# Performance work log

Hardware: AMD Instinct MI355X
Metric: run time of the kernel (lower is better)

## Reference

```python
import math
import jax, jax.numpy as jnp
import numpy as np

H = 12   # num attention heads
DH = 64  # head dim
K = 2    # pooling kernel
ST = 2   # pooling stride


def _alibi_slopes(n):
    def pow2_slopes(n):
        start = 2 ** (-2 ** (-(math.log2(n) - 3)))
        return [start * (start ** i) for i in range(n)]
    if math.log2(n).is_integer():
        return pow2_slopes(n)
    c = 2 ** math.floor(math.log2(n))
    return pow2_slopes(c) + _alibi_slopes(2 * c)[0::2][: n - c]


def _alibi_bias(p, s):
    # [1, H, p, s]; -slope * |i - j|
    rel = np.abs(np.arange(s)[None, :] - np.arange(p)[:, None]).astype(np.float32)
    slopes = np.asarray(_alibi_slopes(H), dtype=np.float32)
    return jnp.asarray((-slopes[:, None, None] * rel[None])[None])


def masked_avg_pool(x, mask):
    # x: [b, S, d] float, mask: [b, S] bool
    b, S, d = x.shape
    pad = (K - S) if K > S else (S - K) % ST
    if pad:
        x = jnp.pad(x, ((0, 0), (0, pad), (0, 0)))
        mask = jnp.pad(mask, ((0, 0), (0, pad)))
    p = (S + pad - K) // ST + 1
    idx = jnp.arange(p)[:, None] * ST + jnp.arange(K)[None, :]  # [p, K]
    xb = x[:, idx]        # [b, p, K, d]
    mb = mask[:, idx]     # [b, p, K]
    norm = jnp.maximum(mb.sum(-1), 1).astype(x.dtype)  # [b, p]
    y = (xb * mb[..., None].astype(x.dtype)).sum(-2) / norm[..., None]
    return y, mb.any(-1)


def setup_inputs() -> dict:
    key = jax.random.key(0)
    k1, k2, k3, k4 = jax.random.split(key, 4)
    B, S, D = 64, 512, 768
    return {
        "hidden_states": jax.random.normal(k1, (B, S, D), dtype=jnp.float32),
        "attention_mask": jax.random.randint(k2, (B, S), 0, 2, dtype=jnp.int32),
        "Wqkv_w": jax.random.normal(k3, (D, 3 * D), dtype=jnp.float32) * 0.02,
        "Wqkv_b": jax.random.normal(k4, (3 * D,), dtype=jnp.float32) * 0.02,
    }


def reference(hidden_states, attention_mask, Wqkv_w, Wqkv_b):
    mask = attention_mask.astype(bool)                    # [b, s]
    b, s, _ = hidden_states.shape
    # fused QKV proj; repad() zeroes padded rows
    qkv = (hidden_states @ Wqkv_w + Wqkv_b) * mask[..., None].astype(hidden_states.dtype)
    q, k, v = jnp.split(qkv, 3, axis=-1)                  # each [b, s, H*DH]
    # masked avg pooling of queries (flattened heads, as in the module)
    q_pooled, new_mask = masked_avg_pool(q, mask)         # [b, p, H*DH], [b, p]
    p = q_pooled.shape[1]
    qh = q_pooled.reshape(b, p, H, DH).transpose(0, 2, 1, 3)  # [b, H, p, DH]
    kh = k.reshape(b, s, H, DH).transpose(0, 2, 1, 3)         # [b, H, s, DH]
    vh = v.reshape(b, s, H, DH).transpose(0, 2, 1, 3)
    # additive bias: 0 where both query and key valid, else -10000; plus ALiBi
    pair = new_mask[:, :, None] & mask[:, None, :]            # [b, p, s]
    bias = jnp.where(pair, 0.0, -10000.0)[:, None] + _alibi_bias(p, s)  # [b, H, p, s]
    scores = jnp.einsum("bhpd,bhsd->bhps", qh, kh) / math.sqrt(DH) + bias
    attn = jax.nn.softmax(scores, axis=-1)
    out = jnp.einsum("bhps,bhsd->bhpd", attn, vh)             # [b, H, p, DH]
    attn_output = out.transpose(0, 2, 1, 3).reshape(b, p, H * DH)
    nm = new_mask[..., None].astype(attn_output.dtype)
    attn_output = attn_output * nm        # emulate unpad(): zero invalid rows
    residual_query = q_pooled * nm
    return attn_output, new_mask, residual_query
```

## Files before the change

kernel.cpp:

```cpp
#include <hip/hip_runtime.h>
#include <cstdint>
#include <cstddef>

#define HH 12
#define DHD 64
#define BB 64
#define SS 512
#define DD 768
#define PP 256
#define N3 2304

typedef __attribute__((ext_vector_type(8))) short bf16x8_t;
typedef __attribute__((ext_vector_type(4))) float f32x4_t;

__constant__ float c_slopes[12] = {
  0.5f, 0.25f, 0.125f, 0.0625f, 0.03125f, 0.015625f, 0.0078125f, 0.00390625f,
  0.70710678118654752f, 0.35355339059327376f, 0.17677669529663688f, 0.08838834764831844f
};

__device__ __forceinline__ ushort f2bf(float f) {
  union { float f; unsigned u; } v; v.f = f;
  unsigned r = v.u + 0x7fffu + ((v.u >> 16) & 1u);
  return (ushort)(r >> 16);
}
__device__ __forceinline__ float bf2f(ushort u) {
  union { unsigned u; float f; } v; v.u = ((unsigned)u) << 16;
  return v.f;
}
__device__ __forceinline__ void gload_lds16(const ushort* g, ushort* l) {
  __builtin_amdgcn_global_load_lds(
      (const __attribute__((address_space(1))) void*)g,
      (__attribute__((address_space(3))) void*)l, 16, 0, 0);
}

__global__ void cast_hs_kernel(const float* __restrict__ in, ushort* __restrict__ out) {
  int i = blockIdx.x * 256 + threadIdx.x;
  float4 v = ((const float4*)in)[i];
  ushort4 o;
  o.x = f2bf(v.x); o.y = f2bf(v.y); o.z = f2bf(v.z); o.w = f2bf(v.w);
  ((ushort4*)out)[i] = o;
}

__global__ void transpose_w_kernel(const float* __restrict__ W, ushort* __restrict__ Wt) {
  __shared__ float tile[32][33];
  int n0 = blockIdx.x * 32, k0 = blockIdx.y * 32;
  int tx = threadIdx.x & 31, ty = threadIdx.x >> 5;
  for (int r = ty; r < 32; r += 8) tile[r][tx] = W[(size_t)(k0 + r) * N3 + n0 + tx];
  __syncthreads();
  for (int r = ty; r < 32; r += 8) Wt[(size_t)(n0 + r) * DD + k0 + tx] = f2bf(tile[tx][r]);
}

__global__ __launch_bounds__(512, 2) void gemm_qkv_kernel(
    const ushort* __restrict__ A, const ushort* __restrict__ Wt,
    const float* __restrict__ bias, const int* __restrict__ mask,
    ushort* __restrict__ qkv) {
  __shared__ __align__(16) ushort As[2][16384];
  __shared__ __align__(16) ushort Bs[2][16384];
  const int wg = blockIdx.x;
  const int swz = (wg & 7) * 144 + (wg >> 3);
  const int bm = (swz / 9) * 256;
  const int bn = (swz % 9) * 256;
  const int tid = threadIdx.x;
  const int lane = tid & 63;
  const int wave = tid >> 6;
  const int wm = (wave >> 2) * 128;
  const int wn = (wave & 3) * 64;
  const int fr = lane & 15, quad = lane >> 4;
  const int xr = (fr & 7) << 3;
  const int q8 = quad * 8;

  const int rsub = tid >> 3;
  const int cg8 = ((tid & 7) ^ (rsub & 7)) * 8;
  const ushort* Ag = A  + (size_t)(bm + rsub) * DD + cg8;
  const ushort* Bg = Wt + (size_t)(bn + rsub) * DD + cg8;
  ushort* AsW = &As[0][0] + wave * 512;
  ushort* BsW = &Bs[0][0] + wave * 512;

  f32x4_t acc[8][4];
#pragma unroll
  for (int i = 0; i < 8; i++)
#pragma unroll
    for (int j = 0; j < 4; j++) acc[i][j] = (f32x4_t){0.f, 0.f, 0.f, 0.f};

#pragma unroll
  for (int l = 0; l < 4; l++) {
    gload_lds16(Ag + (size_t)l * 64 * DD,      AsW + l * 4096);
    gload_lds16(Bg + (size_t)l * 64 * DD,      BsW + l * 4096);
  }
#pragma unroll
  for (int l = 0; l < 4; l++) {
    gload_lds16(Ag + (size_t)l * 64 * DD + 64, AsW + 16384 + l * 4096);
    gload_lds16(Bg + (size_t)l * 64 * DD + 64, BsW + 16384 + l * 4096);
  }
  asm volatile("s_waitcnt vmcnt(8)" ::: "memory");
  __builtin_amdgcn_s_barrier();

#pragma unroll 2
  for (int t = 0; t < 12; t++) {
    const ushort* Ab = &As[t & 1][0];
    const ushort* Bb = &Bs[t & 1][0];
    bf16x8_t a[4][2], b0[2][2], b1[2][2];
#pragma unroll
    for (int m = 0; m < 4; m++)
#pragma unroll
      for (int kk = 0; kk < 2; kk++)
        a[m][kk] = *(const bf16x8_t*)&Ab[(wm + m * 16 + fr) * 64 + ((kk * 32 + q8) ^ xr)];
#pragma unroll
    for (int n = 0; n < 2; n++)
#pragma unroll
      for (int kk = 0; kk < 2; kk++)
        b0[n][kk] = *(const bf16x8_t*)&Bb[(wn + n * 16 + fr) * 64 + ((kk * 32 + q8) ^ xr)];
    asm volatile("" ::: "memory");
    __builtin_amdgcn_s_barrier();
    __builtin_amdgcn_s_setprio(1);
#pragma unroll
    for (int m = 0; m < 4; m++)
#pragma unroll
      for (int n = 0; n < 2; n++) {
        acc[m][n] = __builtin_amdgcn_mfma_f32_16x16x32_bf16(a[m][0], b0[n][0], acc[m][n], 0, 0, 0);
        acc[m][n] = __builtin_amdgcn_mfma_f32_16x16x32_bf16(a[m][1], b0[n][1], acc[m][n], 0, 0, 0);
      }
    __builtin_amdgcn_s_setprio(0);
    __builtin_amdgcn_s_barrier();
#pragma unroll
    for (int n = 0; n < 2; n++)
#pragma unroll
      for (int kk = 0; kk < 2; kk++)
        b1[n][kk] = *(const bf16x8_t*)&Bb[(wn + 32 + n * 16 + fr) * 64 + ((kk * 32 + q8) ^ xr)];
    asm volatile("" ::: "memory");
    __builtin_amdgcn_s_barrier();
    __builtin_amdgcn_s_setprio(1);
#pragma unroll
    for (int m = 0; m < 4; m++)
#pragma unroll
      for (int n = 0; n < 2; n++) {
        acc[m][2 + n] = __builtin_amdgcn_mfma_f32_16x16x32_bf16(a[m][0], b1[n][0], acc[m][2 + n], 0, 0, 0);
        acc[m][2 + n] = __builtin_amdgcn_mfma_f32_16x16x32_bf16(a[m][1], b1[n][1], acc[m][2 + n], 0, 0, 0);
      }
    __builtin_amdgcn_s_setprio(0);
    __builtin_amdgcn_s_barrier();
#pragma unroll
    for (int m = 0; m < 4; m++)
#pragma unroll
      for (int kk = 0; kk < 2; kk++)
        a[m][kk] = *(const bf16x8_t*)&Ab[(wm + 64 + m * 16 + fr) * 64 + ((kk * 32 + q8) ^ xr)];
    asm volatile("" ::: "memory");
    __builtin_amdgcn_s_barrier();
    asm volatile("" ::: "memory");
    if (t < 10) {
      const size_t koff = (size_t)(t + 2) * 64;
      ushort* Ad = AsW + (t & 1) * 16384;
      ushort* Bd = BsW + (t & 1) * 16384;
#pragma unroll
      for (int l = 0; l < 4; l++) {
        gload_lds16(Ag + (size_t)l * 64 * DD + koff, Ad + l * 4096);
        gload_lds16(Bg + (size_t)l * 64 * DD + koff, Bd + l * 4096);
      }
    }
    __builtin_amdgcn_s_setprio(1);
#pragma unroll
    for (int m = 0; m < 4; m++)
#pragma unroll
      for (int n = 0; n < 2; n++) {
        acc[4 + m][n] = __builtin_amdgcn_mfma_f32_16x16x32_bf16(a[m][0], b0[n][0], acc[4 + m][n], 0, 0, 0);
        acc[4 + m][n] = __builtin_amdgcn_mfma_f32_16x16x32_bf16(a[m][1], b0[n][1], acc[4 + m][n], 0, 0, 0);
      }
    __builtin_amdgcn_s_setprio(0);
    __builtin_amdgcn_s_barrier();
    __builtin_amdgcn_s_setprio(1);
#pragma unroll
    for (int m = 0; m < 4; m++)
#pragma unroll
      for (int n = 0; n < 2; n++) {
        acc[4 + m][2 + n] = __builtin_amdgcn_mfma_f32_16x16x32_bf16(a[m][0], b1[n][0], acc[4 + m][2 + n], 0, 0, 0);
        acc[4 + m][2 + n] = __builtin_amdgcn_mfma_f32_16x16x32_bf16(a[m][1], b1[n][1], acc[4 + m][2 + n], 0, 0, 0);
      }
    __builtin_amdgcn_s_setprio(0);
    if (t < 10) { asm volatile("s_waitcnt vmcnt(8)" ::: "memory"); }
    else        { asm volatile("s_waitcnt vmcnt(0)" ::: "memory"); }
    __builtin_amdgcn_s_barrier();
  }

  float bb[4];
#pragma unroll
  for (int j = 0; j < 4; j++) bb[j] = bias[bn + wn + j * 16 + fr];
#pragma unroll
  for (int i = 0; i < 8; i++) {
    const int gm = bm + wm + i * 16 + quad * 4;
#pragma unroll
    for (int r = 0; r < 4; r++) {
      const float mv = (float)mask[gm + r];
      ushort* orow = qkv + (size_t)(gm + r) * N3 + bn + wn + fr;
#pragma unroll
      for (int j = 0; j < 4; j++)
        orow[j * 16] = f2bf((acc[i][j][r] + bb[j]) * mv);
    }
  }
}

__global__ void pool_kernel(const ushort* __restrict__ qkv, const int* __restrict__ mask,
                            float* __restrict__ out, ushort* __restrict__ qp) {
  int idx = blockIdx.x * 256 + threadIdx.x;
  int d4 = idx % 192;
  int bp = idx / 192;
  int b = bp >> 8, p = bp & 255;
  int m0 = mask[b*512 + 2*p], m1 = mask[b*512 + 2*p + 1];
  int ms = m0 + m1;
  float inv = 1.0f / (float)(ms < 1 ? 1 : ms);
  const ushort* r0 = qkv + (size_t)(b*512 + 2*p) * N3 + d4*4;
  ushort4 x0 = *(const ushort4*)r0;
  ushort4 x1 = *(const ushort4*)(r0 + N3);
  float y0 = (bf2f(x0.x) + bf2f(x1.x)) * inv;
  float y1 = (bf2f(x0.y) + bf2f(x1.y)) * inv;
  float y2 = (bf2f(x0.z) + bf2f(x1.z)) * inv;
  float y3 = (bf2f(x0.w) + bf2f(x1.w)) * inv;
  float4 y = {y0, y1, y2, y3};
  *(float4*)(out + 12599296 + (size_t)bp * 768 + d4*4) = y;
  ushort4 q8;
  q8.x = f2bf(y0 * 0.125f); q8.y = f2bf(y1 * 0.125f);
  q8.z = f2bf(y2 * 0.125f); q8.w = f2bf(y3 * 0.125f);
  *(ushort4*)(qp + (size_t)bp * 768 + d4*4) = q8;
  if (d4 == 0) out[12582912 + bp] = (ms > 0) ? 1.0f : 0.0f;
}

__global__ __launch_bounds__(512, 2) void attn_kernel(
    const ushort* __restrict__ qkv, const ushort* __restrict__ qp,
    const int* __restrict__ mask, const float* __restrict__ nmask,
    float* __restrict__ outA) {
  __shared__ __align__(16) ushort K_lds[512 * 64];
  __shared__ __align__(16) ushort VT_lds[64 * 512];
  __shared__ __align__(16) ushort P_lds[8][32][40];
  __shared__ __align__(16) float  kb[512];
  const int h = blockIdx.x, b = blockIdx.y;
  const int tid = threadIdx.x, wave = tid >> 6, lane = tid & 63;
  const int fr = lane & 15, quad = lane >> 4;
  const int kxor = (fr & 7) << 4;
  const float slope = c_slopes[h];

  {
    const int r0 = lane >> 3;
    const int cg = ((lane & 7) ^ r0) * 8;
    const ushort* Ks = qkv + (size_t)(b * 512 + wave * 64 + r0) * N3 + 768 + h * 64 + cg;
#pragma unroll
    for (int i = 0; i < 8; i++)
      gload_lds16(Ks + (size_t)i * 8 * N3, K_lds + (wave * 64 + i * 8) * 64);
  }
  {
    const ushort* Vs = qkv + (size_t)(b * 512 + tid) * N3 + 1536 + h * 64;
    float4 vr[8];
#pragma unroll
    for (int d0 = 0; d0 < 8; d0++) vr[d0] = *(const float4*)(Vs + d0 * 8);
    const int s2 = tid * 2;
    const int sbase = (s2 & ~15), slo = (s2 & 15);
#pragma unroll
    for (int d0 = 0; d0 < 8; d0++) {
      ushort tmp[8];
      *(float4*)tmp = vr[d0];
#pragma unroll
      for (int j = 0; j < 8; j++) {
        int d = d0 * 8 + j;
        *(ushort*)((char*)VT_lds + (size_t)d * 1024 + ((sbase ^ ((d & 7) << 4)) + slo)) = tmp[j];
      }
    }
  }
  kb[tid] = mask[b * 512 + tid] ? 0.0f : -10000.0f;
  bf16x8_t qf[2][2];
#pragma unroll
  for (int nt = 0; nt < 2; nt++)
#pragma unroll
    for (int ks = 0; ks < 2; ks++)
      qf[nt][ks] = *(const bf16x8_t*)(qp + (size_t)(b * 256 + wave * 32 + nt * 16 + fr) * 768
                                      + h * 64 + ks * 32 + quad * 8);
  __syncthreads();

  const char* Kc = (const char*)K_lds;
  const char* Vc = (const char*)VT_lds;
  char* Pw = (char*)&P_lds[wave][0][0];

  f32x4_t O[2][4];
#pragma unroll
  for (int i = 0; i < 2; i++)
#pragma unroll
    for (int j = 0; j < 4; j++) O[i][j] = (f32x4_t){0.f, 0.f, 0.f, 0.f};
  float m_run[2] = {-3.0e38f, -3.0e38f};
  float l_run[2] = {0.f, 0.f};

  for (int sb = 0; sb < 512; sb += 64) {
    f32x4_t sacc[4][2];
#pragma unroll
    for (int mt = 0; mt < 4; mt++) { sacc[mt][0] = (f32x4_t){0,0,0,0}; sacc[mt][1] = (f32x4_t){0,0,0,0}; }
#pragma unroll
    for (int ks = 0; ks < 2; ks++)
#pragma unroll
      for (int mt = 0; mt < 4; mt++) {
        bf16x8_t ak = *(const bf16x8_t*)(Kc + (size_t)(sb + mt * 16 + fr) * 128
                                         + ((ks * 64 + quad * 16) ^ kxor));
        sacc[mt][0] = __builtin_amdgcn_mfma_f32_16x16x32_bf16(ak, qf[0][ks], sacc[mt][0], 0, 0, 0);
        sacc[mt][1] = __builtin_amdgcn_mfma_f32_16x16x32_bf16(ak, qf[1][ks], sacc[mt][1], 0, 0, 0);
      }
    float kbv[4][4];
#pragma unroll
    for (int mt = 0; mt < 4; mt++) {
      f32x4_t kv = *(const f32x4_t*)&kb[sb + mt * 16 + quad * 4];
#pragma unroll
      for (int r = 0; r < 4; r++) kbv[mt][r] = kv[r];
    }
    float pv2[2][4][4];
    float fsv[2];
#pragma unroll
    for (int nt = 0; nt < 2; nt++) {
      const float pidx = (float)(wave * 32 + nt * 16 + fr);
      float mx = -3.0e38f;
#pragma unroll
      for (int mt = 0; mt < 4; mt++)
#pragma unroll
        for (int r = 0; r < 4; r++) {
          float s_ = (float)(sb + mt * 16 + quad * 4 + r);
          float v = sacc[mt][nt][r] + kbv[mt][r] - slope * fabsf(s_ - pidx);
          pv2[nt][mt][r] = v;
          mx = fmaxf(mx, v);
        }
      mx = fmaxf(mx, __shfl_xor(mx, 16, 64));
      mx = fmaxf(mx, __shfl_xor(mx, 32, 64));
      float mnew = fmaxf(m_run[nt], mx);
      float f = __expf(m_run[nt] - mnew);
      m_run[nt] = mnew; fsv[nt] = f;
      float rs = 0.f;
#pragma unroll
      for (int mt = 0; mt < 4; mt++)
#pragma unroll
        for (int r = 0; r < 4; r++) {
          float e = __expf(pv2[nt][mt][r] - mnew);
          pv2[nt][mt][r] = e; rs += e;
        }
      rs += __shfl_xor(rs, 16, 64);
      rs += __shfl_xor(rs, 32, 64);
      l_run[nt] = l_run[nt] * f + rs;
    }
#pragma unroll
    for (int mp = 0; mp < 2; mp++)
#pragma unroll
      for (int r = 0; r < 4; r++) {
        float fb = __shfl(fsv[mp], quad * 4 + r, 64);
#pragma unroll
        for (int nd = 0; nd < 4; nd++) O[mp][nd][r] *= fb;
      }
#pragma unroll
    for (int c = 0; c < 2; c++) {
#pragma unroll
      for (int nt = 0; nt < 2; nt++)
#pragma unroll
        for (int mm = 0; mm < 2; mm++) {
          int mt = c * 2 + mm;
          ushort4 pk;
          pk.x = f2bf(pv2[nt][mt][0]); pk.y = f2bf(pv2[nt][mt][1]);
          pk.z = f2bf(pv2[nt][mt][2]); pk.w = f2bf(pv2[nt][mt][3]);
          *(ushort4*)(Pw + (nt * 16 + fr) * 80 + mm * 32 + quad * 8) = pk;
        }
      bf16x8_t ap0 = *(const bf16x8_t*)(Pw + fr * 80 + quad * 16);
      bf16x8_t ap1 = *(const bf16x8_t*)(Pw + (16 + fr) * 80 + quad * 16);
#pragma unroll
      for (int nd = 0; nd < 4; nd++) {
        bf16x8_t bv = *(const bf16x8_t*)(Vc + (size_t)(nd * 16 + fr) * 1024
                                         + (((sb + c * 32) * 2 + quad * 16) ^ kxor));
        O[0][nd] = __builtin_amdgcn_mfma_f32_16x16x32_bf16(ap0, bv, O[0][nd], 0, 0, 0);
        O[1][nd] = __builtin_amdgcn_mfma_f32_16x16x32_bf16(ap1, bv, O[1][nd], 0, 0, 0);
      }
    }
  }

#pragma unroll
  for (int mp = 0; mp < 2; mp++) {
    const int p0 = wave * 32 + mp * 16 + quad * 4;
#pragma unroll
    for (int r = 0; r < 4; r++) {
      float lb = __shfl(l_run[mp], quad * 4 + r, 64);
      float nm = nmask[b * 256 + p0 + r];
      float scl = nm / lb;
#pragma unroll
      for (int nd = 0; nd < 4; nd++)
        outA[(size_t)(b * 256 + p0 + r) * 768 + h * 64 + nd * 16 + fr] = O[mp][nd][r] * scl;
    }
  }
}

extern "C" void kernel_launch(void* const* d_in, const int* in_sizes, int n_in,
                              void* d_out, int out_size, void* d_ws, size_t ws_size,
                              hipStream_t stream) {
  const float* hs   = (const float*)d_in[0];
  const int*   mask = (const int*)d_in[1];
  const float* W    = (const float*)d_in[2];
  const float* bias = (const float*)d_in[3];
  float* out = (float*)d_out;
  char* ws = (char*)d_ws;
  ushort* A   = (ushort*)(ws);
  ushort* Wt  = (ushort*)(ws + 50331648);
  ushort* qkv = (ushort*)(ws + 53870592);
  ushort* qp  = (ushort*)(ws);

  hipLaunchKernelGGL(cast_hs_kernel, dim3(24576), dim3(256), 0, stream, hs, A);
  hipLaunchKernelGGL(transpose_w_kernel, dim3(72, 24), dim3(256), 0, stream, W, Wt);
  hipLaunchKernelGGL(gemm_qkv_kernel, dim3(1152), dim3(512), 0, stream, A, Wt, bias, mask, qkv);
  hipLaunchKernelGGL(pool_kernel, dim3(12288), dim3(256), 0, stream, qkv, mask, out, qp);
  hipLaunchKernelGGL(attn_kernel, dim3(12, 64), dim3(512), 0, stream,
                     qkv, qp, mask, out + 12582912, out);
}
```

Before: 416.2 us.

## Merge cast and weight-transpose kernels; simplify GEMM inner-loop barrier schedule

Folds the hidden-state bf16 cast and the weight transpose/cast into one launch, using a block-index split, so one kernel launch and its tail are removed. The GEMM main loop drops the fine-grained ping-pong schedule, which had several barriers per K-step and setprio around each MFMA group. It now loads all B fragments at once, issues the two MFMA halves back to back, and synchronises once before prefetching the next stage. This costs more registers for B fragments and less interleaving of LDS reads with MFMAs, in exchange for fewer barriers.

```diff
diff --git a/kernel.cpp b/kernel.cpp
--- a/kernel.cpp
+++ b/kernel.cpp
@@ -33,21 +33,25 @@
       (__attribute__((address_space(3))) void*)l, 16, 0, 0);
 }
 
-__global__ void cast_hs_kernel(const float* __restrict__ in, ushort* __restrict__ out) {
-  int i = blockIdx.x * 256 + threadIdx.x;
-  float4 v = ((const float4*)in)[i];
-  ushort4 o;
-  o.x = f2bf(v.x); o.y = f2bf(v.y); o.z = f2bf(v.z); o.w = f2bf(v.w);
-  ((ushort4*)out)[i] = o;
-}
-
-__global__ void transpose_w_kernel(const float* __restrict__ W, ushort* __restrict__ Wt) {
-  __shared__ float tile[32][33];
-  int n0 = blockIdx.x * 32, k0 = blockIdx.y * 32;
-  int tx = threadIdx.x & 31, ty = threadIdx.x >> 5;
-  for (int r = ty; r < 32; r += 8) tile[r][tx] = W[(size_t)(k0 + r) * N3 + n0 + tx];
-  __syncthreads();
-  for (int r = ty; r < 32; r += 8) Wt[(size_t)(n0 + r) * DD + k0 + tx] = f2bf(tile[tx][r]);
+__global__ __launch_bounds__(256) void prep_kernel(const float* __restrict__ in,
+                                                   ushort* __restrict__ out,
+                                                   const float* __restrict__ W,
+                                                   ushort* __restrict__ Wt) {
+  if (blockIdx.x < 24576) {
+    int i = blockIdx.x * 256 + threadIdx.x;
+    float4 v = ((const float4*)in)[i];
+    ushort4 o;
+    o.x = f2bf(v.x); o.y = f2bf(v.y); o.z = f2bf(v.z); o.w = f2bf(v.w);
+    ((ushort4*)out)[i] = o;
+  } else {
+    __shared__ float tile[32][33];
+    int tb = blockIdx.x - 24576;
+    int n0 = (tb % 72) * 32, k0 = (tb / 72) * 32;
+    int tx = threadIdx.x & 31, ty = threadIdx.x >> 5;
+    for (int r = ty; r < 32; r += 8) tile[r][tx] = W[(size_t)(k0 + r) * N3 + n0 + tx];
+    __syncthreads();
+    for (int r = ty; r < 32; r += 8) Wt[(size_t)(n0 + r) * DD + k0 + tx] = f2bf(tile[tx][r]);
+  }
 }
 
 __global__ __launch_bounds__(512, 2) void gemm_qkv_kernel(
@@ -94,59 +98,45 @@
   }
   asm volatile("s_waitcnt vmcnt(8)" ::: "memory");
   __builtin_amdgcn_s_barrier();
+  asm volatile("" ::: "memory");
 
 #pragma unroll 2
   for (int t = 0; t < 12; t++) {
     const ushort* Ab = &As[t & 1][0];
     const ushort* Bb = &Bs[t & 1][0];
-    bf16x8_t a[4][2], b0[2][2], b1[2][2];
+    bf16x8_t a[4][2], b[4][2];
 #pragma unroll
     for (int m = 0; m < 4; m++)
 #pragma unroll
       for (int kk = 0; kk < 2; kk++)
         a[m][kk] = *(const bf16x8_t*)&Ab[(wm + m * 16 + fr) * 64 + ((kk * 32 + q8) ^ xr)];
 #pragma unroll
-    for (int n = 0; n < 2; n++)
+    for (int n = 0; n < 4; n++)
 #pragma unroll
       for (int kk = 0; kk < 2; kk++)
-        b0[n][kk] = *(const bf16x8_t*)&Bb[(wn + n * 16 + fr) * 64 + ((kk * 32 + q8) ^ xr)];
-    asm volatile("" ::: "memory");
-    __builtin_amdgcn_s_barrier();
-    __builtin_amdgcn_s_setprio(1);
+        b[n][kk] = *(const bf16x8_t*)&Bb[(wn + n * 16 + fr) * 64 + ((kk * 32 + q8) ^ xr)];
 #pragma unroll
     for (int m = 0; m < 4; m++)
 #pragma unroll
-      for (int n = 0; n < 2; n++) {
-        acc[m][n] = __builtin_amdgcn_mfma_f32_16x16x32_bf16(a[m][0], b0[n][0], acc[m][n], 0, 0, 0);
-        acc[m][n] = __builtin_amdgcn_mfma_f32_16x16x32_bf16(a[m][1], b0[n][1], acc[m][n], 0, 0, 0);
-      }
-    __builtin_amdgcn_s_setprio(0);
-    __builtin_amdgcn_s_barrier();
-#pragma unroll
-    for (int n = 0; n < 2; n++)
-#pragma unroll
-      for (int kk = 0; kk < 2; kk++)
-        b1[n][kk] = *(const bf16x8_t*)&Bb[(wn + 32 + n * 16 + fr) * 64 + ((kk * 32 + q8) ^ xr)];
-    asm volatile("" ::: "memory");
-    __builtin_amdgcn_s_barrier();
-    __builtin_amdgcn_s_setprio(1);
-#pragma unroll
-    for (int m = 0; m < 4; m++)
-#pragma unroll
-      for (int n = 0; n < 2; n++) {
-        acc[m][2 + n] = __builtin_amdgcn_mfma_f32_16x16x32_bf16(a[m][0], b1[n][0], acc[m][2 + n], 0, 0, 0);
-        acc[m][2 + n] = __builtin_amdgcn_mfma_f32_16x16x32_bf16(a[m][1], b1[n][1], acc[m][2 + n], 0, 0, 0);
-      }
-    __builtin_amdgcn_s_setprio(0);
-    __builtin_amdgcn_s_barrier();
+      for (int n = 0; n < 4; n++) {
+        acc[m][n] = __builtin_amdgcn_mfma_f32_16x16x32_bf16(a[m][0], b[n][0], acc[m][n], 0, 0, 0);
+        acc[m][n] = __builtin_amdgcn_mfma_f32_16x16x32_bf16(a[m][1], b[n][1], acc[m][n], 0, 0, 0);
+      }
 #pragma unroll
     for (int m = 0; m < 4; m++)
 #pragma unroll
       for (int kk = 0; kk < 2; kk++)
         a[m][kk] = *(const bf16x8_t*)&Ab[(wm + 64 + m * 16 + fr) * 64 + ((kk * 32 + q8) ^ xr)];
-    asm volatile("" ::: "memory");
+#pragma unroll
+    for (int m = 0; m < 4; m++)
+#pragma unroll
+      for (int n = 0; n < 4; n++) {
+        acc[4 + m][n] = __builtin_amdgcn_mfma_f32_16x16x32_bf16(a[m][0], b[n][0], acc[4 + m][n], 0, 0, 0);
+        acc[4 + m][n] = __builtin_amdgcn_mfma_f32_16x16x32_bf16(a[m][1], b[n][1], acc[4 + m][n], 0, 0, 0);
+      }
+    asm volatile("s_waitcnt lgkmcnt(0)" ::: "memory");
+    __builtin_amdgcn_sched_barrier(0);
     __builtin_amdgcn_s_barrier();
-    asm volatile("" ::: "memory");
     if (t < 10) {
       const size_t koff = (size_t)(t + 2) * 64;
       ushort* Ad = AsW + (t & 1) * 16384;
@@ -156,29 +146,12 @@
         gload_lds16(Ag + (size_t)l * 64 * DD + koff, Ad + l * 4096);
         gload_lds16(Bg + (size_t)l * 64 * DD + koff, Bd + l * 4096);
       }
-    }
-    __builtin_amdgcn_s_setprio(1);
-#pragma unroll
-    for (int m = 0; m < 4; m++)
-#pragma unroll
-      for (int n = 0; n < 2; n++) {
-        acc[4 + m][n] = __builtin_amdgcn_mfma_f32_16x16x32_bf16(a[m][0], b0[n][0], acc[4 + m][n], 0, 0, 0);
-        acc[4 + m][n] = __builtin_amdgcn_mfma_f32_16x16x32_bf16(a[m][1], b0[n][1], acc[4 + m][n], 0, 0, 0);
-      }
-    __builtin_amdgcn_s_setprio(0);
+      asm volatile("s_waitcnt vmcnt(8)" ::: "memory");
+    } else {
+      asm volatile("s_waitcnt vmcnt(0)" ::: "memory");
+    }
     __builtin_amdgcn_s_barrier();
-    __builtin_amdgcn_s_setprio(1);
-#pragma unroll
-    for (int m = 0; m < 4; m++)
-#pragma unroll
-      for (int n = 0; n < 2; n++) {
-        acc[4 + m][2 + n] = __builtin_amdgcn_mfma_f32_16x16x32_bf16(a[m][0], b1[n][0], acc[4 + m][2 + n], 0, 0, 0);
-        acc[4 + m][2 + n] = __builtin_amdgcn_mfma_f32_16x16x32_bf16(a[m][1], b1[n][1], acc[4 + m][2 + n], 0, 0, 0);
-      }
-    __builtin_amdgcn_s_setprio(0);
-    if (t < 10) { asm volatile("s_waitcnt vmcnt(8)" ::: "memory"); }
-    else        { asm volatile("s_waitcnt vmcnt(0)" ::: "memory"); }
-    __builtin_amdgcn_s_barrier();
+    asm volatile("" ::: "memory");
   }
 
   float bb[4];
@@ -398,8 +371,7 @@
   ushort* qkv = (ushort*)(ws + 53870592);
   ushort* qp  = (ushort*)(ws);
 
-  hipLaunchKernelGGL(cast_hs_kernel, dim3(24576), dim3(256), 0, stream, hs, A);
-  hipLaunchKernelGGL(transpose_w_kernel, dim3(72, 24), dim3(256), 0, stream, W, Wt);
+  hipLaunchKernelGGL(prep_kernel, dim3(26304), dim3(256), 0, stream, hs, A, W, Wt);
   hipLaunchKernelGGL(gemm_qkv_kernel, dim3(1152), dim3(512), 0, stream, A, Wt, bias, mask, qkv);
   hipLaunchKernelGGL(pool_kernel, dim3(12288), dim3(256), 0, stream, qkv, mask, out, qp);
   hipLaunchKernelGGL(attn_kernel, dim3(12, 64), dim3(512), 0, stream,
```

New measurement: 414.5 us. About the same (-0.4%).
